# Kernel optimization log

Measured on AMD Instinct MI355X. Metric: run time of the kernel, lower is better.

Reference implementation:

```python
import jax, jax.numpy as jnp
import numpy as np
from jax import lax

HIDDEN = 512
EPS = 1e-5


def _conv(x, w):
    # NCHW conv, 3x3, SAME padding, no bias (padding = kernel_size // 2 == 1)
    return lax.conv_general_dilated(
        x, w, window_strides=(1, 1), padding='SAME',
        dimension_numbers=('NCHW', 'OIHW', 'NCHW'))


def setup_inputs() -> dict:
    key = jax.random.key(0)
    ks = jax.random.split(key, 5)
    N, C, H, W = 32, HIDDEN, 32, 32
    fan = C * 9
    std = float(1.0 / np.sqrt(fan))
    return {
        'x': jax.random.normal(ks[0], (N, C, H, W), jnp.float32),
        'w_q': jax.random.normal(ks[1], (C, C, 3, 3), jnp.float32) * std,
        'w_k': jax.random.normal(ks[2], (C, C, 3, 3), jnp.float32) * std,
        'w_v': jax.random.normal(ks[3], (C, C, 3, 3), jnp.float32) * std,
        'w_o': jax.random.normal(ks[4], (C, C, 3, 3), jnp.float32) * std,
        'gamma': jnp.ones((C,), jnp.float32),
        'beta': jnp.zeros((C,), jnp.float32),
    }


def reference(x, w_q, w_k, w_v, w_o, gamma, beta):
    C = x.shape[1]
    q = _conv(x, w_q)  # [N,C,H,W]
    k = _conv(x, w_k)
    v = _conv(x, w_v)
    # (query.unsqueeze(1) * key.unsqueeze(0)).sum(2) == channel contraction
    att = jnp.einsum('ichw,jchw->ijhw', q, k) / jnp.sqrt(jnp.asarray(C, x.dtype))
    att = jax.nn.softmax(att, axis=1)  # softmax over key instances
    virt = jnp.einsum('ijhw,jchw->ichw', att, v)  # [N,C,H,W]
    # GroupNorm(1, C): normalize over (C,H,W) per instance, per-channel affine
    mean = jnp.mean(virt, axis=(1, 2, 3), keepdims=True)
    var = jnp.var(virt, axis=(1, 2, 3), keepdims=True)
    virt = (virt - mean) * lax.rsqrt(var + EPS)
    virt = virt * gamma[None, :, None, None] + beta[None, :, None, None]
    virt = jax.nn.relu(virt)
    virt = _conv(virt, w_o)
    # Dropout(0.2) is identity in eval mode
    return x + virt
```

## Files before the change

kernel.cpp:

```cpp
#include <hip/hip_runtime.h>

namespace {

constexpr int kN  = 32;
constexpr int kC  = 512;
constexpr int kH  = 32;
constexpr int kW  = 32;
constexpr int kHW = kH * kW;

constexpr int PCH   = 36992;
constexpr size_t WTF_ELEMS = (size_t)9 * kC * kC;
constexpr size_t XH_ELEMS  = (size_t)kN * 16 * PCH;
constexpr size_t QKV_ELEMS = (size_t)kN * kHW * kC;

using bf16x8 = __attribute__((ext_vector_type(8))) short;
using bf16x4 = __attribute__((ext_vector_type(4))) short;
using f32x4  = __attribute__((ext_vector_type(4))) float;

__device__ __forceinline__ float bf2f(short s) {
  unsigned u = ((unsigned)(unsigned short)s) << 16;
  return __builtin_bit_cast(float, u);
}
__device__ __forceinline__ short f2bf(float f) {
  unsigned u = __builtin_bit_cast(unsigned, f);
  u += 0x7FFFu + ((u >> 16) & 1u);
  return (short)(u >> 16);
}
__device__ __forceinline__ void gload_lds16(const void* g, void* l) {
  __builtin_amdgcn_global_load_lds(
      (const __attribute__((address_space(1))) void*)g,
      (__attribute__((address_space(3))) void*)l, 16, 0, 0);
}

__global__ __launch_bounds__(256) void wtf_pack_kernel(
    const float* __restrict__ wq, const float* __restrict__ wk,
    const float* __restrict__ wv, const float* __restrict__ wo,
    short* __restrict__ oq, short* __restrict__ ok,
    short* __restrict__ ov, short* __restrict__ oo) {
  const float* wsrc[4] = {wq, wk, wv, wo};
  short* wdst[4] = {oq, ok, ov, oo};
  const float* w = wsrc[blockIdx.z];
  short* wtf = wdst[blockIdx.z];
  __shared__ float tile[32][289];
  const int co0 = blockIdx.x * 32;
  const int ci0 = blockIdx.y * 32;
  for (int idx = threadIdx.x; idx < 32 * 288; idx += 256) {
    int c = idx % 288, r = idx / 288;
    tile[r][c] = w[(size_t)(co0 + r) * (kC * 9) + (size_t)ci0 * 9 + c];
  }
  __syncthreads();
  const int kkb  = ci0 >> 5;
  const int nnG0 = co0 >> 4;
  for (int g = threadIdx.x; g < 9 * 2 * 64; g += 256) {
    int laneg = g & 63;
    int nnL   = (g >> 6) & 1;
    int t     = g >> 7;
    int hi    = laneg >> 4;
    int coL   = nnL * 16 + (laneg & 15);
    bf16x8 pk;
#pragma unroll
    for (int j = 0; j < 8; ++j) pk[j] = f2bf(tile[coL][(hi * 8 + j) * 9 + t]);
    *(bf16x8*)&wtf[(((size_t)t * 16 + kkb) * 32 + nnG0 + nnL) * 512 + laneg * 8] = pk;
  }
}

__global__ __launch_bounds__(256) void x2xh_kernel(
    const float* __restrict__ x, short* __restrict__ xh) {
  __shared__ float tile[32][33];
  const int ch = blockIdx.x;
  const int h  = blockIdx.y;
  const int n  = blockIdx.z;
  const int w0 = threadIdx.x & 31;
  const int c0 = threadIdx.x >> 5;
#pragma unroll
  for (int pass = 0; pass < 4; ++pass) {
    int cir = pass * 8 + c0;
    tile[w0][cir] = x[(((size_t)n * kC + ch * 32 + cir) * kH + h) * kW + w0];
  }
  __syncthreads();
  const int wv = threadIdx.x >> 3;
  const int g4 = (threadIdx.x & 7) * 4;
  bf16x4 pk;
#pragma unroll
  for (int j = 0; j < 4; ++j) pk[j] = f2bf(tile[wv][g4 + j]);
  *(bf16x4*)&xh[(((size_t)n * 16 + ch) * 1156 + (size_t)(h + 1) * 34 + (wv + 1)) * 32 + g4] = pk;
}

__global__ __launch_bounds__(256, 2) void conv_qkv_kernel(
    const short* __restrict__ xin,
    const short* __restrict__ wtq, const short* __restrict__ wtk,
    const short* __restrict__ wtv,
    short* __restrict__ outq, short* __restrict__ outk,
    short* __restrict__ outv) {
  __shared__ __align__(16) short As[3][8192];
  const int tid  = threadIdx.x;
  const int lane = tid & 63;
  const int l15  = lane & 15, lhi = lane >> 4;
  const int w    = tid >> 6;
  const int wbase = tid & 192;

  const int xcd = blockIdx.x & 7;
  const int m   = blockIdx.x >> 3;
  const int co0 = (m >> 5) * 64;
  const int spt = m & 7;
  const int n   = xcd * 4 + ((m >> 3) & 3);
  const int h0  = spt * 4;
  const int sp0 = spt * 128;

  const short* srcA = xin + (size_t)n * (16 * PCH) + (size_t)h0 * (34 * 32);
  const size_t boff = ((size_t)(co0 >> 4) + w) * 512 + lane * 8;
  const short* bp[3] = {wtq + boff, wtk + boff, wtv + boff};

  f32x4 acc[3][8];
#pragma unroll
  for (int c = 0; c < 3; ++c)
#pragma unroll
    for (int mf = 0; mf < 8; ++mf)
#pragma unroll
      for (int r = 0; r < 4; ++r) acc[c][mf][r] = 0.f;

#define STAGE_A(kk, buf)                                                      \
  {                                                                           \
    const short* gA = srcA + (size_t)(kk) * PCH;                              \
    _Pragma("unroll") for (int pass = 0; pass < 4; ++pass)                    \
        gload_lds16(gA + (size_t)(pass * 256 + tid) * 8,                      \
                    &As[buf][(pass * 256 + wbase) * 8]);                      \
  }

  STAGE_A(0, 0);
  STAGE_A(1, 1);
  bf16x8 cur[3], nxt[3];
#pragma unroll
  for (int j = 0; j < 3; ++j)
    cur[j] = *(const bf16x8*)&bp[j][0];

  int ab = 0;
  int sb = 2;
  for (int kk = 0; kk < 16; ++kk) {
    asm volatile("s_waitcnt vmcnt(7)" ::: "memory");
    __builtin_amdgcn_s_barrier();
#pragma unroll
    for (int t = 0; t < 9; ++t) {
      {
        const int nt  = (t < 8) ? (t + 1) : 0;
        const int nkk = (t < 8) ? kk : kk + 1;
        const size_t bo = (size_t)(nt * 16 + nkk) * 16384;
#pragma unroll
        for (int j = 0; j < 3; ++j)
          nxt[j] = *(const bf16x8*)&bp[j][bo];
      }
      if (t == 1 && kk < 14) STAGE_A(kk + 2, sb);
      const int dy = t / 3, dx = t % 3;
      bf16x8 a[8];
#pragma unroll
      for (int mf = 0; mf < 8; ++mf) {
        const int pb = ((mf >> 1) + dy) * 34 + (mf & 1) * 16 + l15 + dx;
        a[mf] = *(const bf16x8*)&As[ab][pb * 32 + lhi * 8];
      }
      __builtin_amdgcn_s_setprio(1);
#pragma unroll
      for (int c = 0; c < 3; ++c)
#pragma unroll
        for (int mf = 0; mf < 8; ++mf)
          acc[c][mf] = __builtin_amdgcn_mfma_f32_16x16x32_bf16(
              a[mf], cur[c], acc[c][mf], 0, 0, 0);
      __builtin_amdgcn_s_setprio(0);
#pragma unroll
      for (int j = 0; j < 3; ++j) cur[j] = nxt[j];
    }
    ab = (ab == 2) ? 0 : ab + 1;
    sb = (sb == 2) ? 0 : sb + 1;
  }
#undef STAGE_A

  short* outs[3] = {outq, outk, outv};
#pragma unroll
  for (int c = 0; c < 3; ++c) {
    short* out = outs[c];
#pragma unroll
    for (int mf = 0; mf < 8; ++mf)
#pragma unroll
      for (int r = 0; r < 4; ++r) {
        size_t off = ((size_t)n * kHW + sp0 + mf * 16 + lhi * 4 + r) * kC
                     + co0 + w * 16 + l15;
        out[off] = f2bf(acc[c][mf][r]);
      }
  }
}

__global__ __launch_bounds__(256, 3) void conv_o_kernel(
    const short* __restrict__ xin, const short* __restrict__ wtf,
    const float* __restrict__ xres, float* __restrict__ out) {
  __shared__ __align__(16) short As[3][8192];
  const int tid  = threadIdx.x;
  const int lane = tid & 63;
  const int l15  = lane & 15, lhi = lane >> 4;
  const int wv   = tid >> 6;
  const int wm   = wv >> 1, wn = wv & 1;
  const int wbase = tid & 192;

  const int xcd = blockIdx.x & 7;
  const int m   = blockIdx.x >> 3;
  const int co0 = (m >> 5) * 128;
  const int spt = m & 7;
  const int n   = xcd * 4 + ((m >> 3) & 3);
  const int h0  = spt * 4;
  const int sp0 = spt * 128;

  const short* srcA = xin + (size_t)n * (16 * PCH) + (size_t)h0 * (34 * 32);
  const short* bptr = wtf + ((size_t)(co0 >> 4) + wn * 4) * 512 + lane * 8;

  f32x4 acc[4][4];
#pragma unroll
  for (int mf = 0; mf < 4; ++mf)
#pragma unroll
    for (int nf = 0; nf < 4; ++nf)
#pragma unroll
      for (int r = 0; r < 4; ++r) acc[mf][nf][r] = 0.f;

#define STAGE_A(kk, buf)                                                      \
  {                                                                           \
    const short* gA = srcA + (size_t)(kk) * PCH;                              \
    _Pragma("unroll") for (int pass = 0; pass < 4; ++pass)                    \
        gload_lds16(gA + (size_t)(pass * 256 + tid) * 8,                      \
                    &As[buf][(pass * 256 + wbase) * 8]);                      \
  }

  STAGE_A(0, 0);
  STAGE_A(1, 1);
  bf16x8 cur[4], nxt[4];
#pragma unroll
  for (int j = 0; j < 4; ++j)
    cur[j] = *(const bf16x8*)&bptr[(size_t)j * 512];

  int ab = 0, sb = 2;
  for (int kk = 0; kk < 16; ++kk) {
    asm volatile("s_waitcnt vmcnt(8)" ::: "memory");
    __builtin_amdgcn_s_barrier();
#pragma unroll
    for (int t = 0; t < 9; ++t) {
      {
        const int nt  = (t < 8) ? (t + 1) : 0;
        const int nkk = (t < 8) ? kk : kk + 1;
        const size_t bo = (size_t)(nt * 16 + nkk) * 16384;
#pragma unroll
        for (int j = 0; j < 4; ++j)
          nxt[j] = *(const bf16x8*)&bptr[bo + (size_t)j * 512];
      }
      if (t == 1 && kk < 14) STAGE_A(kk + 2, sb);
      const int dy = t / 3, dx = t % 3;
      bf16x8 a[4];
#pragma unroll
      for (int mf = 0; mf < 4; ++mf) {
        const int pb = (wm * 2 + (mf >> 1) + dy) * 34 + (mf & 1) * 16 + l15 + dx;
        a[mf] = *(const bf16x8*)&As[ab][pb * 32 + lhi * 8];
      }
      __builtin_amdgcn_s_setprio(1);
#pragma unroll
      for (int mf = 0; mf < 4; ++mf)
#pragma unroll
        for (int nf = 0; nf < 4; ++nf)
          acc[mf][nf] = __builtin_amdgcn_mfma_f32_16x16x32_bf16(
              a[mf], cur[nf], acc[mf][nf], 0, 0, 0);
      __builtin_amdgcn_s_setprio(0);
#pragma unroll
      for (int j = 0; j < 4; ++j) cur[j] = nxt[j];
    }
    ab = (ab == 2) ? 0 : ab + 1;
    sb = (sb == 2) ? 0 : sb + 1;
  }
#undef STAGE_A

  float* T = (float*)&As[0][0];
#pragma unroll
  for (int nf = 0; nf < 4; ++nf) {
    __syncthreads();
    const int coL = wn * 16 + l15;
#pragma unroll
    for (int mf = 0; mf < 4; ++mf)
#pragma unroll
      for (int r = 0; r < 4; ++r)
        T[coL * 129 + wm * 64 + mf * 16 + lhi * 4 + r] = acc[mf][nf][r];
    __syncthreads();
#pragma unroll
    for (int it = 0; it < 16; ++it) {
      int idx = it * 256 + tid;
      int c = idx >> 7, sp = idx & 127;
      int co = co0 + (c >> 4) * 64 + nf * 16 + (c & 15);
      size_t off = ((size_t)n * kC + co) * kHW + sp0 + sp;
      out[off] = T[c * 129 + sp] + xres[off];
    }
  }
}

__global__ __launch_bounds__(256) void attn_mfma_kernel(
    const short* q, const short* __restrict__ k,
    const short* __restrict__ v, short* virt, float* __restrict__ gsum) {
  __shared__ __align__(16) short Qs[32 * 72];
  __shared__ __align__(16) short Ks[32 * 72];
  __shared__ __align__(16) float Ps[32 * 36];
  __shared__ __align__(16) short Vt[64 * 40];
  const int p    = blockIdx.x;
  const int tid  = threadIdx.x;
  const int lane = tid & 63;
  const int l15  = lane & 15, lhi = lane >> 4;
  const int w    = tid >> 6;
  const int iq   = w >> 1, jq = w & 1;

  f32x4 accS = {0.f, 0.f, 0.f, 0.f};
  const int si = tid >> 3;
  const int sc = (tid & 7) * 8;
  for (int c0 = 0; c0 < kC; c0 += 64) {
    __syncthreads();
    {
      size_t g = ((size_t)si * kHW + p) * kC + c0 + sc;
      *(bf16x8*)&Qs[si * 72 + sc] = *(const bf16x8*)&q[g];
      *(bf16x8*)&Ks[si * 72 + sc] = *(const bf16x8*)&k[g];
    }
    __syncthreads();
#pragma unroll
    for (int cs = 0; cs < 2; ++cs) {
      bf16x8 aq = *(const bf16x8*)&Qs[(iq * 16 + l15) * 72 + cs * 32 + lhi * 8];
      bf16x8 bk = *(const bf16x8*)&Ks[(jq * 16 + l15) * 72 + cs * 32 + lhi * 8];
      accS = __builtin_amdgcn_mfma_f32_16x16x32_bf16(aq, bk, accS, 0, 0, 0);
    }
  }
  __syncthreads();
  constexpr float scale = 0.044194173824159216f;
#pragma unroll
  for (int r = 0; r < 4; ++r)
    Ps[(iq * 16 + lhi * 4 + r) * 36 + jq * 16 + l15] = accS[r] * scale;
  __syncthreads();

  {
    const int i  = tid >> 3;
    const int j0 = (tid & 7) * 4;
    float a0 = Ps[i * 36 + j0], a1 = Ps[i * 36 + j0 + 1];
    float a2 = Ps[i * 36 + j0 + 2], a3 = Ps[i * 36 + j0 + 3];
    float mx = fmaxf(fmaxf(a0, a1), fmaxf(a2, a3));
    for (int off = 1; off < 8; off <<= 1) mx = fmaxf(mx, __shfl_xor(mx, off));
    float e0 = __expf(a0 - mx), e1 = __expf(a1 - mx);
    float e2 = __expf(a2 - mx), e3 = __expf(a3 - mx);
    float s = e0 + e1 + e2 + e3;
    for (int off = 1; off < 8; off <<= 1) s += __shfl_xor(s, off);
    const float inv = 1.f / s;
    Ps[i * 36 + j0]     = e0 * inv;
    Ps[i * 36 + j0 + 1] = e1 * inv;
    Ps[i * 36 + j0 + 2] = e2 * inv;
    Ps[i * 36 + j0 + 3] = e3 * inv;
  }
  __syncthreads();

  bf16x8 ap[2];
#pragma unroll
  for (int it = 0; it < 2; ++it) {
    const float* pr = &Ps[(it * 16 + l15) * 36 + lhi * 8];
    float4 lo = *(const float4*)pr;
    float4 hi4 = *(const float4*)(pr + 4);
    ap[it][0] = f2bf(lo.x);  ap[it][1] = f2bf(lo.y);
    ap[it][2] = f2bf(lo.z);  ap[it][3] = f2bf(lo.w);
    ap[it][4] = f2bf(hi4.x); ap[it][5] = f2bf(hi4.y);
    ap[it][6] = f2bf(hi4.z); ap[it][7] = f2bf(hi4.w);
  }
  __syncthreads();

  float gs[8], gq2[8];
#pragma unroll
  for (int idx = 0; idx < 8; ++idx) { gs[idx] = 0.f; gq2[idx] = 0.f; }

  const f32x4 zacc = {0.f, 0.f, 0.f, 0.f};
  for (int c0 = 0; c0 < kC; c0 += 64) {
    __syncthreads();
    {
      const int j = tid >> 3, c8g = tid & 7;
      bf16x8 vvv = *(const bf16x8*)&v[((size_t)j * kHW + p) * kC + c0 + c8g * 8];
#pragma unroll
      for (int jj = 0; jj < 8; ++jj) {
        int c = c8g * 8 + jj;
        int byte = (c * 80 + j * 2) ^ (((c >> 3) & 7) << 4);
        *(short*)((char*)Vt + byte) = vvv[jj];
      }
    }
    __syncthreads();
    {
      const int c = w * 16 + l15;
      const int byte = (c * 80 + lhi * 16) ^ (((c >> 3) & 7) << 4);
      bf16x8 bv = *(const bf16x8*)((const char*)Vt + byte);
#pragma unroll
      for (int it = 0; it < 2; ++it) {
        f32x4 o = __builtin_amdgcn_mfma_f32_16x16x32_bf16(ap[it], bv, zacc, 0, 0, 0);
#pragma unroll
        for (int r = 0; r < 4; ++r) {
          short ob = f2bf(o[r]);
          virt[((size_t)(it * 16 + lhi * 4 + r) * kHW + p) * kC + c0 + w * 16 + l15] = ob;
          float fv = bf2f(ob);
          gs[it * 4 + r] += fv;
          gq2[it * 4 + r] = fmaf(fv, fv, gq2[it * 4 + r]);
        }
      }
    }
  }

#pragma unroll
  for (int idx = 0; idx < 8; ++idx)
    for (int off = 1; off < 16; off <<= 1) {
      gs[idx]  += __shfl_xor(gs[idx], off);
      gq2[idx] += __shfl_xor(gq2[idx], off);
    }
  __syncthreads();
  float* SS = Ps;
  if (l15 == 0) {
#pragma unroll
    for (int idx = 0; idx < 8; ++idx) {
      int it = idx >> 2, r = idx & 3;
      int i = it * 16 + lhi * 4 + r;
      SS[(w * 32 + i) * 2]     = gs[idx];
      SS[(w * 32 + i) * 2 + 1] = gq2[idx];
    }
  }
  __syncthreads();
  if (tid < 32) {
    float s = 0.f, q2 = 0.f;
#pragma unroll
    for (int ww = 0; ww < 4; ++ww) {
      s  += SS[(ww * 32 + tid) * 2];
      q2 += SS[(ww * 32 + tid) * 2 + 1];
    }
    atomicAdd(&gsum[tid], s);
    atomicAdd(&gsum[32 + tid], q2);
  }
}

__global__ __launch_bounds__(64) void gn_final_kernel(
    const float* __restrict__ gsum, float* __restrict__ stats) {
  if (threadIdx.x < 32) {
    constexpr float invn = 1.f / ((float)kHW * kC);
    float mean = gsum[threadIdx.x] * invn;
    float var = gsum[32 + threadIdx.x] * invn - mean * mean;
    stats[threadIdx.x] = mean;
    stats[32 + threadIdx.x] = rsqrtf(var + 1e-5f);
  }
}

__global__ __launch_bounds__(256) void gn_apply_kernel(
    const short* __restrict__ virt, const float* __restrict__ stats,
    const float* __restrict__ gamma, const float* __restrict__ beta,
    short* __restrict__ vh) {
  const size_t g = (size_t)blockIdx.x * 256 + threadIdx.x;
  const int i    = (int)(g >> 16);
  const int rest = (int)(g & 65535);
  const int p    = rest >> 6;
  const int c8g  = rest & 63;
  const int ci   = c8g * 8;
  const float mean = stats[i];
  const float rstd = stats[32 + i];
  bf16x8 vv = *(const bf16x8*)&virt[((size_t)i * kHW + p) * kC + ci];
  const float4 ga = ((const float4*)gamma)[c8g * 2];
  const float4 gb = ((const float4*)gamma)[c8g * 2 + 1];
  const float4 ba = ((const float4*)beta)[c8g * 2];
  const float4 bb = ((const float4*)beta)[c8g * 2 + 1];
  const float gv[8] = {ga.x, ga.y, ga.z, ga.w, gb.x, gb.y, gb.z, gb.w};
  const float bv[8] = {ba.x, ba.y, ba.z, ba.w, bb.x, bb.y, bb.z, bb.w};
  bf16x8 o;
#pragma unroll
  for (int jj = 0; jj < 8; ++jj) {
    float f = (bf2f(vv[jj]) - mean) * rstd;
    f = fmaxf(fmaf(f, gv[jj], bv[jj]), 0.f);
    o[jj] = f2bf(f);
  }
  const size_t dst =
      (((size_t)i * 16 + (ci >> 5)) * 1156 + (size_t)((p >> 5) + 1) * 34 + (p & 31) + 1) * 32
      + (ci & 31);
  *(bf16x8*)&vh[dst] = o;
}

}

extern "C" void kernel_launch(void* const* d_in, const int* in_sizes, int n_in,
                              void* d_out, int out_size, void* d_ws,
                              size_t ws_size, hipStream_t stream) {
  const float* x     = (const float*)d_in[0];
  const float* w_q   = (const float*)d_in[1];
  const float* w_k   = (const float*)d_in[2];
  const float* w_v   = (const float*)d_in[3];
  const float* w_o   = (const float*)d_in[4];
  const float* gamma = (const float*)d_in[5];
  const float* beta  = (const float*)d_in[6];

  short* ws    = (short*)d_ws;
  short* wtf_q = ws;
  short* wtf_k = wtf_q + WTF_ELEMS;
  short* wtf_v = wtf_k + WTF_ELEMS;
  short* wtf_o = wtf_v + WTF_ELEMS;
  short* xh    = wtf_o + WTF_ELEMS;
  short* vh    = xh + XH_ELEMS;
  short* qb    = vh + XH_ELEMS;
  short* kb    = qb + QKV_ELEMS;
  short* vb    = kb + QKV_ELEMS;
  float* stats = (float*)(vb + QKV_ELEMS);
  float* gsum  = stats + 64;
  short* virt  = qb;
  hipMemsetAsync(xh, 0, (size_t)2 * XH_ELEMS * sizeof(short), stream);
  hipMemsetAsync(gsum, 0, 64 * sizeof(float), stream);

  wtf_pack_kernel<<<dim3(16, 16, 4), 256, 0, stream>>>(
      w_q, w_k, w_v, w_o, wtf_q, wtf_k, wtf_v, wtf_o);

  x2xh_kernel<<<dim3(16, 32, 32), 256, 0, stream>>>(x, xh);

  conv_qkv_kernel<<<2048, 256, 0, stream>>>(xh, wtf_q, wtf_k, wtf_v,
                                            qb, kb, vb);

  attn_mfma_kernel<<<kHW, 256, 0, stream>>>(qb, kb, vb, virt, gsum);

  gn_final_kernel<<<1, 64, 0, stream>>>(gsum, stats);
  gn_apply_kernel<<<(int)(QKV_ELEMS / 8 / 256), 256, 0, stream>>>(
      virt, stats, gamma, beta, vh);

  conv_o_kernel<<<1024, 256, 0, stream>>>(vh, wtf_o, x, (float*)d_out);
}
```

Measured before the change: 563.6 us.

## Zero only halo borders, trim QKV conv registers, rewarp output conv tiling

New measurement: 553.3 us. About the same (-1.8%).

```diff
diff --git a/kernel.cpp b/kernel.cpp
--- a/kernel.cpp
+++ b/kernel.cpp
@@ -86,7 +86,26 @@
   *(bf16x4*)&xh[(((size_t)n * 16 + ch) * 1156 + (size_t)(h + 1) * 34 + (wv + 1)) * 32 + g4] = pk;
 }
 
-__global__ __launch_bounds__(256, 2) void conv_qkv_kernel(
+__global__ __launch_bounds__(256) void halo_zero_kernel(
+    short* __restrict__ xh, short* __restrict__ vh) {
+  short* base = (blockIdx.x & 1) ? vh : xh;
+  const int plane = blockIdx.x >> 1;
+  short* dst = base + (size_t)plane * PCH;
+  const int t = threadIdx.x;
+  if (t < 132) {
+    int row, col;
+    if (t < 34)       { row = 0;          col = t; }
+    else if (t < 68)  { row = 33;         col = t - 34; }
+    else if (t < 100) { row = t - 68 + 1; col = 0; }
+    else              { row = t - 100 + 1; col = 33; }
+    const bf16x8 z = {0, 0, 0, 0, 0, 0, 0, 0};
+    short* q = dst + (size_t)(row * 34 + col) * 32;
+#pragma unroll
+    for (int j = 0; j < 4; ++j) *(bf16x8*)&q[j * 8] = z;
+  }
+}
+
+__global__ __launch_bounds__(256, 3) void conv_qkv_kernel(
     const short* __restrict__ xin,
     const short* __restrict__ wtq, const short* __restrict__ wtk,
     const short* __restrict__ wtv,
@@ -129,7 +148,7 @@
 
   STAGE_A(0, 0);
   STAGE_A(1, 1);
-  bf16x8 cur[3], nxt[3];
+  bf16x8 cur[3];
 #pragma unroll
   for (int j = 0; j < 3; ++j)
     cur[j] = *(const bf16x8*)&bp[j][0];
@@ -141,14 +160,6 @@
     __builtin_amdgcn_s_barrier();
 #pragma unroll
     for (int t = 0; t < 9; ++t) {
-      {
-        const int nt  = (t < 8) ? (t + 1) : 0;
-        const int nkk = (t < 8) ? kk : kk + 1;
-        const size_t bo = (size_t)(nt * 16 + nkk) * 16384;
-#pragma unroll
-        for (int j = 0; j < 3; ++j)
-          nxt[j] = *(const bf16x8*)&bp[j][bo];
-      }
       if (t == 1 && kk < 14) STAGE_A(kk + 2, sb);
       const int dy = t / 3, dx = t % 3;
       bf16x8 a[8];
@@ -157,16 +168,19 @@
         const int pb = ((mf >> 1) + dy) * 34 + (mf & 1) * 16 + l15 + dx;
         a[mf] = *(const bf16x8*)&As[ab][pb * 32 + lhi * 8];
       }
-      __builtin_amdgcn_s_setprio(1);
-#pragma unroll
-      for (int c = 0; c < 3; ++c)
+      const int nt  = (t < 8) ? (t + 1) : 0;
+      const int nkk = (t < 8) ? kk : kk + 1;
+      const size_t bo = (size_t)(nt * 16 + nkk) * 16384;
+#pragma unroll
+      for (int c = 0; c < 3; ++c) {
+        __builtin_amdgcn_s_setprio(1);
 #pragma unroll
         for (int mf = 0; mf < 8; ++mf)
           acc[c][mf] = __builtin_amdgcn_mfma_f32_16x16x32_bf16(
               a[mf], cur[c], acc[c][mf], 0, 0, 0);
-      __builtin_amdgcn_s_setprio(0);
-#pragma unroll
-      for (int j = 0; j < 3; ++j) cur[j] = nxt[j];
+        __builtin_amdgcn_s_setprio(0);
+        cur[c] = *(const bf16x8*)&bp[c][bo];
+      }
     }
     ab = (ab == 2) ? 0 : ab + 1;
     sb = (sb == 2) ? 0 : sb + 1;
@@ -195,8 +209,7 @@
   const int tid  = threadIdx.x;
   const int lane = tid & 63;
   const int l15  = lane & 15, lhi = lane >> 4;
-  const int wv   = tid >> 6;
-  const int wm   = wv >> 1, wn = wv & 1;
+  const int w    = tid >> 6;
   const int wbase = tid & 192;
 
   const int xcd = blockIdx.x & 7;
@@ -208,15 +221,15 @@
   const int sp0 = spt * 128;
 
   const short* srcA = xin + (size_t)n * (16 * PCH) + (size_t)h0 * (34 * 32);
-  const short* bptr = wtf + ((size_t)(co0 >> 4) + wn * 4) * 512 + lane * 8;
-
-  f32x4 acc[4][4];
-#pragma unroll
-  for (int mf = 0; mf < 4; ++mf)
-#pragma unroll
-    for (int nf = 0; nf < 4; ++nf)
-#pragma unroll
-      for (int r = 0; r < 4; ++r) acc[mf][nf][r] = 0.f;
+  const short* bptr = wtf + ((size_t)(co0 >> 4) + w * 2) * 512 + lane * 8;
+
+  f32x4 acc[2][8];
+#pragma unroll
+  for (int nf = 0; nf < 2; ++nf)
+#pragma unroll
+    for (int mf = 0; mf < 8; ++mf)
+#pragma unroll
+      for (int r = 0; r < 4; ++r) acc[nf][mf][r] = 0.f;
 
 #define STAGE_A(kk, buf)                                                      \
   {                                                                           \
@@ -228,14 +241,14 @@
 
   STAGE_A(0, 0);
   STAGE_A(1, 1);
-  bf16x8 cur[4], nxt[4];
-#pragma unroll
-  for (int j = 0; j < 4; ++j)
+  bf16x8 cur[2], nxt[2];
+#pragma unroll
+  for (int j = 0; j < 2; ++j)
     cur[j] = *(const bf16x8*)&bptr[(size_t)j * 512];
 
   int ab = 0, sb = 2;
   for (int kk = 0; kk < 16; ++kk) {
-    asm volatile("s_waitcnt vmcnt(8)" ::: "memory");
+    asm volatile("s_waitcnt vmcnt(6)" ::: "memory");
     __builtin_amdgcn_s_barrier();
 #pragma unroll
     for (int t = 0; t < 9; ++t) {
@@ -244,27 +257,27 @@
         const int nkk = (t < 8) ? kk : kk + 1;
         const size_t bo = (size_t)(nt * 16 + nkk) * 16384;
 #pragma unroll
-        for (int j = 0; j < 4; ++j)
+        for (int j = 0; j < 2; ++j)
           nxt[j] = *(const bf16x8*)&bptr[bo + (size_t)j * 512];
       }
       if (t == 1 && kk < 14) STAGE_A(kk + 2, sb);
       const int dy = t / 3, dx = t % 3;
-      bf16x8 a[4];
-#pragma unroll
-      for (int mf = 0; mf < 4; ++mf) {
-        const int pb = (wm * 2 + (mf >> 1) + dy) * 34 + (mf & 1) * 16 + l15 + dx;
+      bf16x8 a[8];
+#pragma unroll
+      for (int mf = 0; mf < 8; ++mf) {
+        const int pb = ((mf >> 1) + dy) * 34 + (mf & 1) * 16 + l15 + dx;
         a[mf] = *(const bf16x8*)&As[ab][pb * 32 + lhi * 8];
       }
       __builtin_amdgcn_s_setprio(1);
 #pragma unroll
-      for (int mf = 0; mf < 4; ++mf)
-#pragma unroll
-        for (int nf = 0; nf < 4; ++nf)
-          acc[mf][nf] = __builtin_amdgcn_mfma_f32_16x16x32_bf16(
-              a[mf], cur[nf], acc[mf][nf], 0, 0, 0);
+      for (int nf = 0; nf < 2; ++nf)
+#pragma unroll
+        for (int mf = 0; mf < 8; ++mf)
+          acc[nf][mf] = __builtin_amdgcn_mfma_f32_16x16x32_bf16(
+              a[mf], cur[nf], acc[nf][mf], 0, 0, 0);
       __builtin_amdgcn_s_setprio(0);
 #pragma unroll
-      for (int j = 0; j < 4; ++j) cur[j] = nxt[j];
+      for (int j = 0; j < 2; ++j) cur[j] = nxt[j];
     }
     ab = (ab == 2) ? 0 : ab + 1;
     sb = (sb == 2) ? 0 : sb + 1;
@@ -273,22 +286,22 @@
 
   float* T = (float*)&As[0][0];
 #pragma unroll
-  for (int nf = 0; nf < 4; ++nf) {
+  for (int nf = 0; nf < 2; ++nf) {
     __syncthreads();
-    const int coL = wn * 16 + l15;
-#pragma unroll
-    for (int mf = 0; mf < 4; ++mf)
+    const int tr = w * 16 + l15;
+#pragma unroll
+    for (int mf = 0; mf < 8; ++mf)
 #pragma unroll
       for (int r = 0; r < 4; ++r)
-        T[coL * 129 + wm * 64 + mf * 16 + lhi * 4 + r] = acc[mf][nf][r];
+        T[tr * 129 + mf * 16 + lhi * 4 + r] = acc[nf][mf][r];
     __syncthreads();
 #pragma unroll
-    for (int it = 0; it < 16; ++it) {
+    for (int it = 0; it < 32; ++it) {
       int idx = it * 256 + tid;
-      int c = idx >> 7, sp = idx & 127;
-      int co = co0 + (c >> 4) * 64 + nf * 16 + (c & 15);
+      int trr = idx >> 7, sp = idx & 127;
+      int co = co0 + (trr >> 4) * 32 + nf * 16 + (trr & 15);
       size_t off = ((size_t)n * kC + co) * kHW + sp0 + sp;
-      out[off] = T[c * 129 + sp] + xres[off];
+      out[off] = T[trr * 129 + sp] + xres[off];
     }
   }
 }
@@ -500,7 +513,7 @@
   float* stats = (float*)(vb + QKV_ELEMS);
   float* gsum  = stats + 64;
   short* virt  = qb;
-  hipMemsetAsync(xh, 0, (size_t)2 * XH_ELEMS * sizeof(short), stream);
+  halo_zero_kernel<<<1024, 256, 0, stream>>>(xh, vh);
   hipMemsetAsync(gsum, 0, 64 * sizeof(float), stream);
 
   wtf_pack_kernel<<<dim3(16, 16, 4), 256, 0, stream>>>(
```
